# Performance work log

Hardware: AMD Instinct MI355X
Metric: run time of the kernel (lower is better)

The kernel has to match this reference:

```python
import jax, jax.numpy as jnp
import numpy as np

B, C_IN, H, W = 4, 512, 188, 188
SHARED_CH = 64
NUM_CLASS = 3
M = 200
NUM_MAX = 500
STRIDE = 8
PCR = (-75.2, -75.2, -2.0, 75.2, 75.2, 4.0)
VOX = (0.1, 0.1, 0.15)
OUT_CH = (2, 1, 3, 2, 1, 3)  # center, center_z, dim, rot, iou, hm
MIN_RADIUS = 2.0
OVERLAP = 0.1
INIT_BIAS = -2.19


def conv3x3(x, w):
    return jax.lax.conv_general_dilated(x, w, (1, 1), 'SAME',
                                        dimension_numbers=('NCHW', 'OIHW', 'NCHW'))


def bn_relu(x, p):
    # p: [4, C] = gamma, beta, running_mean, running_var (inference-mode BN)
    g, b, m, v = p[0], p[1], p[2], p[3]
    scale = (g * jax.lax.rsqrt(v + 1e-5))[None, :, None, None]
    y = (x - m[None, :, None, None]) * scale + b[None, :, None, None]
    return jax.nn.relu(y)


def gaussian_radius(height, width, min_overlap):
    # Faithful to OpenPCDet centernet_utils.gaussian_radius
    b1 = height + width
    c1 = width * height * (1 - min_overlap) / (1 + min_overlap)
    sq1 = jnp.sqrt(jnp.maximum(b1 * b1 - 4.0 * c1, 0.0))
    r1 = (b1 + sq1) / 2.0
    b2 = 2.0 * (height + width)
    c2 = (1 - min_overlap) * width * height
    sq2 = jnp.sqrt(jnp.maximum(b2 * b2 - 16.0 * c2, 0.0))
    r2 = (b2 + sq2) / 2.0
    a3 = 4.0 * min_overlap
    b3 = -2.0 * min_overlap * (height + width)
    c3 = (min_overlap - 1.0) * width * height
    sq3 = jnp.sqrt(jnp.maximum(b3 * b3 - 4.0 * a3 * c3, 0.0))
    r3 = (b3 + sq3) / 2.0
    return jnp.minimum(jnp.minimum(r1, r2), r3)


def assign_targets(gt_boxes):
    # gt_boxes: [B, M, 8] = x, y, z, dx, dy, dz, heading, class(1..NUM_CLASS)
    x, y, z = gt_boxes[..., 0], gt_boxes[..., 1], gt_boxes[..., 2]
    dx, dy, dz = gt_boxes[..., 3], gt_boxes[..., 4], gt_boxes[..., 5]
    heading = gt_boxes[..., 6]
    cls = jax.lax.stop_gradient(gt_boxes[..., 7]).astype(jnp.int32)

    cx = jnp.clip((x - PCR[0]) / VOX[0] / STRIDE, 0.0, W - 0.5)  # [B,M]
    cy = jnp.clip((y - PCR[1]) / VOX[1] / STRIDE, 0.0, H - 0.5)
    cxi = jax.lax.stop_gradient(jnp.floor(cx)).astype(jnp.int32)  # .int() trunc == floor (>=0)
    cyi = jax.lax.stop_gradient(jnp.floor(cy)).astype(jnp.int32)

    dxp = dx / VOX[0] / STRIDE
    dyp = dy / VOX[1] / STRIDE
    r = gaussian_radius(dxp, dyp, OVERLAP)
    r = jnp.maximum(jnp.floor(jax.lax.stop_gradient(r)), MIN_RADIUS)  # clamp_min(r.int(), 2)
    sigma = (2.0 * r + 1.0) / 6.0
    valid = (dx > 0) & (dy > 0)  # [B,M]

    ox = jnp.arange(W, dtype=jnp.int32)[None, None, :] - cxi[..., None]  # [B,M,W]
    oy = jnp.arange(H, dtype=jnp.int32)[None, None, :] - cyi[..., None]  # [B,M,H]
    d2 = (oy.astype(jnp.float32) ** 2)[:, :, :, None] + (ox.astype(jnp.float32) ** 2)[:, :, None, :]
    g = jnp.exp(-d2 / (2.0 * sigma * sigma)[:, :, None, None])  # [B,M,H,W]
    win = (jnp.abs(oy)[:, :, :, None] <= r[:, :, None, None]) & \
          (jnp.abs(ox)[:, :, None, :] <= r[:, :, None, None])
    g = jnp.where(win & valid[:, :, None, None], g, 0.0)

    # per-class max-splat (draw_gaussian_to_heatmap uses torch.max overlap)
    heatmap = jnp.stack(
        [jnp.max(jnp.where((cls == c + 1)[:, :, None, None], g, 0.0), axis=1)
         for c in range(NUM_CLASS)], axis=1)  # [B,NUM_CLASS,H,W]

    vf = valid.astype(gt_boxes.dtype)
    vals = jnp.stack([cx - cxi.astype(cx.dtype), cy - cyi.astype(cy.dtype), z,
                      jnp.log(dx), jnp.log(dy), jnp.log(dz),
                      jnp.cos(heading), jnp.sin(heading)], axis=-1) * vf[..., None]
    target_boxes = jnp.zeros((B, NUM_MAX, 8), gt_boxes.dtype).at[:, :M].set(vals)
    ind_vals = (cyi * W + cxi) * valid.astype(jnp.int32)
    inds = jnp.zeros((B, NUM_MAX), jnp.int32).at[:, :M].set(ind_vals)
    mask = jnp.zeros((B, NUM_MAX), jnp.int32).at[:, :M].set(valid.astype(jnp.int32))
    return heatmap, target_boxes, inds, mask


def setup_inputs() -> dict:
    key = jax.random.key(0)
    ks = jax.random.split(key, 16)
    spatial_features = jax.random.normal(ks[0], (B, C_IN, H, W), jnp.float32)
    x = jax.random.uniform(ks[1], (B, M), minval=-70.0, maxval=70.0)
    y = jax.random.uniform(ks[2], (B, M), minval=-70.0, maxval=70.0)
    z = jax.random.uniform(ks[3], (B, M), minval=-1.0, maxval=1.0)
    dx = jax.random.uniform(ks[4], (B, M), minval=1.5, maxval=5.0)
    dy = jax.random.uniform(ks[5], (B, M), minval=1.5, maxval=5.0)
    dz = jax.random.uniform(ks[6], (B, M), minval=1.0, maxval=3.0)
    hd = jax.random.uniform(ks[7], (B, M), minval=-np.pi, maxval=np.pi)
    cls = jax.random.randint(ks[8], (B, M), 1, NUM_CLASS + 1).astype(jnp.float32)
    gt_boxes = jnp.stack([x, y, z, dx, dy, dz, hd, cls], axis=-1)

    def mk_bn(k, lead):
        kk = jax.random.split(k, 4)
        g = 1.0 + 0.1 * jax.random.normal(kk[0], lead + (SHARED_CH,))
        b = 0.1 * jax.random.normal(kk[1], lead + (SHARED_CH,))
        m = 0.1 * jax.random.normal(kk[2], lead + (SHARED_CH,))
        v = jax.random.uniform(kk[3], lead + (SHARED_CH,), minval=0.5, maxval=1.5)
        return jnp.stack([g, b, m, v], axis=len(lead))

    w_shared = jax.random.normal(ks[9], (SHARED_CH, C_IN, 3, 3)) * (1.0 / np.sqrt(C_IN * 9))
    bn_shared = mk_bn(ks[10], ())
    w1_heads = jax.random.normal(ks[11], (6, SHARED_CH, SHARED_CH, 3, 3)) * (1.0 / np.sqrt(SHARED_CH * 9))
    bn_heads = mk_bn(ks[12], (6,))
    w2_heads = jax.random.normal(ks[13], (6, 3, SHARED_CH, 3, 3)) * (1.0 / np.sqrt(SHARED_CH * 9))
    b2_heads = jnp.zeros((6, 3), jnp.float32).at[5].set(INIT_BIAS)  # hm branch bias = -2.19
    return {'spatial_features': spatial_features, 'gt_boxes': gt_boxes,
            'w_shared': w_shared, 'bn_shared': bn_shared,
            'w1_heads': w1_heads, 'bn_heads': bn_heads,
            'w2_heads': w2_heads, 'b2_heads': b2_heads}


def reference(spatial_features, gt_boxes, w_shared, bn_shared,
              w1_heads, bn_heads, w2_heads, b2_heads):
    shared = bn_relu(conv3x3(spatial_features, w_shared), bn_shared)  # [B,64,H,W]

    def branch(w1, bnp, w2, b2):
        h = bn_relu(conv3x3(shared, w1), bnp)
        return conv3x3(h, w2) + b2[None, :, None, None]  # [B,3,H,W] (out padded to 3)

    outs = jax.vmap(branch)(w1_heads, bn_heads, w2_heads, b2_heads)  # [6,B,3,H,W]
    head_out = jnp.concatenate([outs[i, :, :OUT_CH[i]] for i in range(6)], axis=1)  # [B,12,H,W]

    heatmap, target_boxes, inds, mask = assign_targets(gt_boxes)
    return head_out, heatmap, target_boxes, inds, mask
```

## Files before the change

### kernel.cpp

```cpp
#include <hip/hip_runtime.h>
#include <hip/hip_bf16.h>

#define HWD 188
#define NPX (HWD*HWD)
#define NB 4
#define CIN 512
#define CH 64
#define MBOX 200
#define NMAX 500

#define HEAD_SZ (NB*12*NPX)
#define HM_OFF  HEAD_SZ
#define TB_OFF  (HM_OFF + NB*3*NPX)
#define IND_OFF (TB_OFF + NB*NMAX*8)
#define MSK_OFF (IND_OFF + NB*NMAX)

typedef short sh8 __attribute__((ext_vector_type(8)));
typedef float f4 __attribute__((ext_vector_type(4)));
typedef unsigned short us4 __attribute__((ext_vector_type(4)));

__device__ __constant__ int d_cum[6]  = {0, 2, 3, 6, 8, 9};
__device__ __constant__ int d_outc[6] = {2, 1, 3, 2, 1, 3};

__device__ __forceinline__ unsigned short bf16_bits(float v) {
  union { __hip_bfloat16 h; unsigned short u; } cv;
  cv.h = __float2bfloat16(v);
  return cv.u;
}

__device__ __forceinline__ int xcd_swz(int bid, int grid) {
  return (bid & 7) * (grid >> 3) + (bid >> 3);
}

__global__ __launch_bounds__(256) void wprep(
    const float* __restrict__ ws_, const float* __restrict__ w1_,
    const float* __restrict__ w2_, unsigned short* __restrict__ w1b,
    unsigned short* __restrict__ w2b, unsigned short* __restrict__ w3b) {
  int e = blockIdx.x * 256 + threadIdx.x;
  const int N1 = 9 * 16 * 64 * 32;
  const int N2 = 6 * 9 * 64 * 64;
  const int N3 = 6 * 9 * 16 * 64;
  if (e < N1) {
    int icr = e & 31; int r1 = e >> 5;
    int oc = r1 & 63; int r2 = r1 >> 6;
    int icq = r2 & 15; int tap = r2 >> 4;
    w1b[e] = bf16_bits(ws_[(oc * 512 + icq * 32 + icr) * 9 + tap]);
  } else if (e < N1 + N2) {
    int f = e - N1;
    int h = f / (9 * 64 * 64); int r = f % (9 * 64 * 64);
    int tap = r / (64 * 64); int r2 = r % (64 * 64);
    int oc = r2 / 64; int ic = r2 % 64;
    w2b[f] = bf16_bits(w1_[((h * 64 + oc) * 64 + ic) * 9 + tap]);
  } else if (e < N1 + N2 + N3) {
    int f = e - N1 - N2;
    int h = f / (9 * 16 * 64); int r = f % (9 * 16 * 64);
    int tap = r / (16 * 64); int r2 = r % (16 * 64);
    int oc = r2 / 64; int ic = r2 % 64;
    float v = (oc < 3) ? w2_[((h * 3 + oc) * 64 + ic) * 9 + tap] : 0.f;
    w3b[f] = bf16_bits(v);
  }
}

#define C1_LDS (10*18*32)
__global__ __launch_bounds__(256, 4) void conv1_mfma(
    const float* __restrict__ sf,
    const unsigned short* __restrict__ wb,
    const float* __restrict__ bnp,
    unsigned short* __restrict__ outp) {
  __shared__ __align__(16) short s_in[2][C1_LDS];
  const int t = threadIdx.x;
  const int swz = xcd_swz(blockIdx.x, 1152);
  const int b = swz / 288;
  const int tt = swz % 288;
  const int y0 = (tt / 12) * 8, x0 = (tt % 12) * 16;
  const int w = t >> 6, lane = t & 63, ln = lane & 15, kg = lane >> 4;
  const int rg = w & 1, og = w >> 1;

  const bool st_act = (t < 240);
  const int icg = t & 3, cg = (t >> 2) % 6, sr = (t >> 2) / 6;
  const int gy_s = y0 - 1 + sr;
  const int gx0_s = x0 - 4 + cg * 4;
  const bool row_ok = (gy_s >= 0 && gy_s < HWD);
  const bool vec_ok = (gx0_s >= 0 && gx0_s + 3 < HWD);
  const float* sbase = sf + (((long long)b * CIN + icg * 8) * HWD + gy_s) * HWD + gx0_s;

  f4 acc[2][4];
#pragma unroll
  for (int i = 0; i < 2; ++i)
#pragma unroll
    for (int j = 0; j < 4; ++j) acc[i][j] = (f4){0.f, 0.f, 0.f, 0.f};

  f4 st[8];
#pragma unroll
  for (int j = 0; j < 8; ++j) st[j] = (f4){0.f, 0.f, 0.f, 0.f};

#define C1_LOAD(IC0)                                                        \
  do {                                                                      \
    if (st_act && row_ok) {                                                 \
      const float* p = sbase + (long long)(IC0) * NPX;                      \
      if (vec_ok) {                                                         \
        _Pragma("unroll")                                                   \
        for (int j = 0; j < 8; ++j)                                         \
          st[j] = *reinterpret_cast<const f4*>(p + (long long)j * NPX);     \
      } else {                                                              \
        _Pragma("unroll")                                                   \
        for (int j = 0; j < 8; ++j) st[j] = (f4){0.f, 0.f, 0.f, 0.f};       \
        _Pragma("unroll")                                                   \
        for (int k = 0; k < 4; ++k) {                                       \
          int gx = gx0_s + k;                                               \
          if (gx >= 0 && gx < HWD) {                                        \
            _Pragma("unroll")                                               \
            for (int j = 0; j < 8; ++j) st[j][k] = p[(long long)j * NPX + k];\
          }                                                                 \
        }                                                                   \
      }                                                                     \
    } else {                                                                \
      _Pragma("unroll")                                                     \
      for (int j = 0; j < 8; ++j) st[j] = (f4){0.f, 0.f, 0.f, 0.f};         \
    }                                                                       \
  } while (0)

#define C1_WRITE(BUF)                                                       \
  do {                                                                      \
    if (st_act) {                                                           \
      _Pragma("unroll")                                                     \
      for (int k = 0; k < 4; ++k) {                                         \
        int col = cg * 4 + k - 3;                                           \
        if ((unsigned)col < 18u) {                                          \
          sh8 pk;                                                           \
          _Pragma("unroll")                                                 \
          for (int j = 0; j < 8; ++j) pk[j] = (short)bf16_bits(st[j][k]);   \
          *reinterpret_cast<sh8*>(&(BUF)[(sr * 18 + col) * 32 + icg * 8]) = pk; \
        }                                                                   \
      }                                                                     \
    }                                                                       \
  } while (0)

  C1_LOAD(0);
  C1_WRITE(s_in[0]);
  __syncthreads();

  for (int s = 0; s < 16; ++s) {
    const short* cur = s_in[s & 1];
    if (s < 15) C1_LOAD((s + 1) * 32);
#pragma unroll
    for (int tap = 0; tap < 9; ++tap) {
      const int ky = tap / 3, kx = tap % 3;
      sh8 af[2];
#pragma unroll
      for (int i = 0; i < 2; ++i)
        af[i] = *reinterpret_cast<const sh8*>(
            wb + (((tap * 16 + s) * 64) + (2 * og + i) * 16 + ln) * 32 + kg * 8);
#pragma unroll
      for (int nt = 0; nt < 4; ++nt) {
        const int rr = 4 * rg + nt + ky;
        const int cc = ln + kx;
        sh8 bf = *reinterpret_cast<const sh8*>(&cur[(rr * 18 + cc) * 32 + kg * 8]);
#pragma unroll
        for (int i = 0; i < 2; ++i)
          acc[i][nt] = __builtin_amdgcn_mfma_f32_16x16x32_bf16(
              af[i], bf, acc[i][nt], 0, 0, 0);
      }
    }
    if (s < 15) C1_WRITE(s_in[(s & 1) ^ 1]);
    __syncthreads();
  }

#pragma unroll
  for (int i = 0; i < 2; ++i) {
    const int ocb = (2 * og + i) * 16 + kg * 4;
    f4 g4 = *reinterpret_cast<const f4*>(bnp + ocb);
    f4 b4 = *reinterpret_cast<const f4*>(bnp + 64 + ocb);
    f4 m4 = *reinterpret_cast<const f4*>(bnp + 128 + ocb);
    f4 v4 = *reinterpret_cast<const f4*>(bnp + 192 + ocb);
    f4 sc, bi;
#pragma unroll
    for (int j = 0; j < 4; ++j) {
      sc[j] = g4[j] * rsqrtf(v4[j] + 1e-5f);
      bi[j] = b4[j] - m4[j] * sc[j];
    }
#pragma unroll
    for (int nt = 0; nt < 4; ++nt) {
      int y = y0 + 4 * rg + nt;
      int x = x0 + ln;
      if (y < HWD && x < HWD) {
        us4 pk;
#pragma unroll
        for (int j = 0; j < 4; ++j)
          pk[j] = bf16_bits(fmaxf(acc[i][nt][j] * sc[j] + bi[j], 0.f));
        *reinterpret_cast<us4*>(outp + (((long long)b * HWD + y) * HWD + x) * 64 + ocb) = pk;
      }
    }
  }
#undef C1_LOAD
#undef C1_WRITE
}

__global__ __launch_bounds__(256, 3) void conv2_allheads(
    const unsigned short* __restrict__ inp,
    const unsigned short* __restrict__ w2b,
    const float* __restrict__ bnH,
    unsigned short* __restrict__ tmp0,
    int h_lo, int h_hi, long long tstride) {
  __shared__ __align__(16) short s_in[10 * 34 * 72];
  const int t = threadIdx.x;
  const int swz = xcd_swz(blockIdx.x, gridDim.x);
  const int b = swz / 144;
  const int tt = swz % 144;
  const int y0 = (tt / 6) * 8, x0 = (tt % 6) * 32;
  const int w = t >> 6, lane = t & 63, ln = lane & 15, kg = lane >> 4;

  for (int idx = t; idx < 2720; idx += 256) {
    int ch = idx & 7; int pix = idx >> 3;
    int c = pix % 34; int r = pix / 34;
    int gy = y0 - 1 + r, gx = x0 - 1 + c;
    sh8 v = (sh8){0, 0, 0, 0, 0, 0, 0, 0};
    if (gy >= 0 && gy < HWD && gx >= 0 && gx < HWD)
      v = *reinterpret_cast<const sh8*>(
          &inp[(((long long)b * HWD + gy) * HWD + gx) * 64 + ch * 8]);
    *reinterpret_cast<sh8*>(&s_in[(r * 34 + c) * 72 + ch * 8]) = v;
  }
  __syncthreads();

  for (int h = h_lo; h < h_hi; ++h) {
    f4 acc[4][4];
#pragma unroll
    for (int i = 0; i < 4; ++i)
#pragma unroll
      for (int j = 0; j < 4; ++j) acc[i][j] = (f4){0.f, 0.f, 0.f, 0.f};
#pragma unroll
    for (int icq = 0; icq < 2; ++icq) {
#pragma unroll
      for (int tap = 0; tap < 9; ++tap) {
        const int ky = tap / 3, kx = tap % 3;
        sh8 af[4];
#pragma unroll
        for (int ot = 0; ot < 4; ++ot)
          af[ot] = *reinterpret_cast<const sh8*>(
              w2b + (((h * 9 + tap) * 64) + ot * 16 + ln) * 64 + icq * 32 + kg * 8);
#pragma unroll
        for (int nt = 0; nt < 4; ++nt) {
          const int rr = 2 * w + (nt >> 1) + ky;
          const int cc = (nt & 1) * 16 + ln + kx;
          sh8 bf = *reinterpret_cast<const sh8*>(
              &s_in[(rr * 34 + cc) * 72 + icq * 32 + kg * 8]);
#pragma unroll
          for (int ot = 0; ot < 4; ++ot)
            acc[ot][nt] = __builtin_amdgcn_mfma_f32_16x16x32_bf16(
                af[ot], bf, acc[ot][nt], 0, 0, 0);
        }
      }
    }
    unsigned short* outp = tmp0 + (long long)h * tstride;
    const float* bnp = bnH + h * 256;
#pragma unroll
    for (int ot = 0; ot < 4; ++ot) {
      const int ocb = ot * 16 + kg * 4;
      f4 g4 = *reinterpret_cast<const f4*>(bnp + ocb);
      f4 b4 = *reinterpret_cast<const f4*>(bnp + 64 + ocb);
      f4 m4 = *reinterpret_cast<const f4*>(bnp + 128 + ocb);
      f4 v4 = *reinterpret_cast<const f4*>(bnp + 192 + ocb);
      f4 sc, bi;
#pragma unroll
      for (int j = 0; j < 4; ++j) {
        sc[j] = g4[j] * rsqrtf(v4[j] + 1e-5f);
        bi[j] = b4[j] - m4[j] * sc[j];
      }
#pragma unroll
      for (int nt = 0; nt < 4; ++nt) {
        int y = y0 + 2 * w + (nt >> 1);
        int x = x0 + (nt & 1) * 16 + ln;
        if (y < HWD && x < HWD) {
          us4 pk;
#pragma unroll
          for (int j = 0; j < 4; ++j)
            pk[j] = bf16_bits(fmaxf(acc[ot][nt][j] * sc[j] + bi[j], 0.f));
          *reinterpret_cast<us4*>(outp + (((long long)b * HWD + y) * HWD + x) * 64 + ocb) = pk;
        }
      }
    }
  }
}

__global__ __launch_bounds__(256, 3) void conv3_mfma(
    const unsigned short* __restrict__ tmp0,
    const unsigned short* __restrict__ w3b,
    const float* __restrict__ b2,
    float* __restrict__ hout,
    int h_base, long long tstride) {
  __shared__ __align__(16) short s_in[10 * 34 * 72];
  const int t = threadIdx.x;
  const int swz = xcd_swz(blockIdx.x, gridDim.x);
  const int h = h_base + swz / 576;
  const int rem = swz % 576;
  const int b = rem / 144;
  const int tt = rem % 144;
  const int y0 = (tt / 6) * 8, x0 = (tt % 6) * 32;
  const int w = t >> 6, lane = t & 63, ln = lane & 15, kg = lane >> 4;
  const unsigned short* inp = tmp0 + (long long)h * tstride;

  for (int idx = t; idx < 2720; idx += 256) {
    int ch = idx & 7; int pix = idx >> 3;
    int c = pix % 34; int r = pix / 34;
    int gy = y0 - 1 + r, gx = x0 - 1 + c;
    sh8 v = (sh8){0, 0, 0, 0, 0, 0, 0, 0};
    if (gy >= 0 && gy < HWD && gx >= 0 && gx < HWD)
      v = *reinterpret_cast<const sh8*>(
          &inp[(((long long)b * HWD + gy) * HWD + gx) * 64 + ch * 8]);
    *reinterpret_cast<sh8*>(&s_in[(r * 34 + c) * 72 + ch * 8]) = v;
  }
  __syncthreads();

  f4 acc[4];
#pragma unroll
  for (int j = 0; j < 4; ++j) acc[j] = (f4){0.f, 0.f, 0.f, 0.f};
#pragma unroll
  for (int icq = 0; icq < 2; ++icq) {
#pragma unroll
    for (int tap = 0; tap < 9; ++tap) {
      const int ky = tap / 3, kx = tap % 3;
      sh8 af = *reinterpret_cast<const sh8*>(
          w3b + (((h * 9 + tap) * 16) + ln) * 64 + icq * 32 + kg * 8);
#pragma unroll
      for (int nt = 0; nt < 4; ++nt) {
        const int rr = 2 * w + (nt >> 1) + ky;
        const int cc = (nt & 1) * 16 + ln + kx;
        sh8 bf = *reinterpret_cast<const sh8*>(
            &s_in[(rr * 34 + cc) * 72 + icq * 32 + kg * 8]);
        acc[nt] = __builtin_amdgcn_mfma_f32_16x16x32_bf16(af, bf, acc[nt], 0, 0, 0);
      }
    }
  }
  const int c_off = d_cum[h], noc = d_outc[h];
#pragma unroll
  for (int nt = 0; nt < 4; ++nt) {
    int y = y0 + 2 * w + (nt >> 1);
    int x = x0 + (nt & 1) * 16 + ln;
    if (y < HWD && x < HWD) {
#pragma unroll
      for (int j = 0; j < 4; ++j) {
        int oc = kg * 4 + j;
        if (oc < noc)
          hout[((long long)b * 12 + c_off + oc) * NPX + y * HWD + x] =
              acc[nt][j] + b2[h * 3 + oc];
      }
    }
  }
}

__global__ __launch_bounds__(256) void targets_kernel(
    const float* __restrict__ gt, float* __restrict__ out, float* __restrict__ boxp) {
  int idx = blockIdx.x * 256 + threadIdx.x;
  if (idx >= NB * NMAX) return;
  int b = idx / NMAX, j = idx - b * NMAX;
  float vals[8] = {0, 0, 0, 0, 0, 0, 0, 0};
  float indf = 0.f, mkf = 0.f;
  if (j < MBOX) {
    const float* g = gt + (b * MBOX + j) * 8;
    float x = g[0], y = g[1], z = g[2], dx = g[3], dy = g[4], dz = g[5];
    float hd = g[6], cls = g[7];
    float cx = (x - (-75.2f)) / 0.1f / 8.0f;
    cx = fminf(fmaxf(cx, 0.0f), (float)HWD - 0.5f);
    float cy = (y - (-75.2f)) / 0.1f / 8.0f;
    cy = fminf(fmaxf(cy, 0.0f), (float)HWD - 0.5f);
    float cxf = floorf(cx), cyf = floorf(cy);
    int cxi = (int)cxf, cyi = (int)cyf;
    float hh = dx / 0.1f / 8.0f;
    float ww = dy / 0.1f / 8.0f;
    const float ov = 0.1f;
    float b1 = hh + ww;
    float c1 = ww * hh * (1.0f - ov) / (1.0f + ov);
    float sq1 = sqrtf(fmaxf(b1 * b1 - 4.0f * c1, 0.0f));
    float r1 = (b1 + sq1) / 2.0f;
    float b2_ = 2.0f * (hh + ww);
    float c2 = (1.0f - ov) * ww * hh;
    float sq2 = sqrtf(fmaxf(b2_ * b2_ - 16.0f * c2, 0.0f));
    float r2 = (b2_ + sq2) / 2.0f;
    float a3 = 4.0f * ov;
    float b3 = -2.0f * ov * (hh + ww);
    float c3 = (ov - 1.0f) * ww * hh;
    float sq3 = sqrtf(fmaxf(b3 * b3 - 4.0f * a3 * c3, 0.0f));
    float r3 = (b3 + sq3) / 2.0f;
    float r = fminf(fminf(r1, r2), r3);
    r = fmaxf(floorf(r), 2.0f);
    float sigma = (2.0f * r + 1.0f) / 6.0f;
    float inv2s2 = 1.0f / (2.0f * sigma * sigma);
    bool valid = (dx > 0.0f) && (dy > 0.0f);
    float vf = valid ? 1.0f : 0.0f;
    vals[0] = (cx - cxf) * vf;
    vals[1] = (cy - cyf) * vf;
    vals[2] = z * vf;
    vals[3] = logf(dx) * vf;
    vals[4] = logf(dy) * vf;
    vals[5] = logf(dz) * vf;
    vals[6] = cosf(hd) * vf;
    vals[7] = sinf(hd) * vf;
    indf = (float)((cyi * HWD + cxi) * (valid ? 1 : 0));
    mkf = vf;
    float* bp = boxp + (b * MBOX + j) * 8;
    bp[0] = cxf; bp[1] = cyf; bp[2] = r; bp[3] = inv2s2;
    bp[4] = valid ? cls : 0.0f; bp[5] = 0.f; bp[6] = 0.f; bp[7] = 0.f;
  }
  float* tb = out + TB_OFF + (b * NMAX + j) * 8;
#pragma unroll
  for (int k = 0; k < 8; ++k) tb[k] = vals[k];
  out[IND_OFF + b * NMAX + j] = indf;
  out[MSK_OFF + b * NMAX + j] = mkf;
}

__global__ __launch_bounds__(256) void heatmap_kernel(
    const float* __restrict__ boxp, float* __restrict__ out) {
  __shared__ float s_bp[MBOX][5];
  const int t = threadIdx.x, b = blockIdx.y;
  for (int e = t; e < MBOX * 5; e += 256) {
    int j = e / 5, k = e - j * 5;
    s_bp[j][k] = boxp[(b * MBOX + j) * 8 + k];
  }
  __syncthreads();
  int p = blockIdx.x * 256 + t;
  if (p >= NPX) return;
  int y = p / HWD, x = p - y * HWD;
  float a0 = 0.f, a1 = 0.f, a2 = 0.f;
  for (int j = 0; j < MBOX; ++j) {
    int c = (int)s_bp[j][4];
    if (c == 0) continue;
    float ox = (float)x - s_bp[j][0];
    float oy = (float)y - s_bp[j][1];
    float r = s_bp[j][2];
    if (fabsf(ox) <= r && fabsf(oy) <= r) {
      float gg = expf(-(ox * ox + oy * oy) * s_bp[j][3]);
      if (c == 1) a0 = fmaxf(a0, gg);
      else if (c == 2) a1 = fmaxf(a1, gg);
      else a2 = fmaxf(a2, gg);
    }
  }
  int base = HM_OFF + (b * 3 * HWD + y) * HWD + x;
  out[base] = a0;
  out[base + NPX] = a1;
  out[base + 2 * NPX] = a2;
}

extern "C" void kernel_launch(void* const* d_in, const int* in_sizes, int n_in,
                              void* d_out, int out_size, void* d_ws, size_t ws_size,
                              hipStream_t stream) {
  (void)in_sizes; (void)n_in; (void)out_size;
  const float* sf = (const float*)d_in[0];
  const float* gt = (const float*)d_in[1];
  const float* w_shared = (const float*)d_in[2];
  const float* bn_shared = (const float*)d_in[3];
  const float* w1 = (const float*)d_in[4];
  const float* bnH = (const float*)d_in[5];
  const float* w2 = (const float*)d_in[6];
  const float* b2 = (const float*)d_in[7];
  float* out = (float*)d_out;
  char* ws = (char*)d_ws;

  const size_t SH = (size_t)NB * NPX * 64 * 2;
  unsigned short* shared_t = (unsigned short*)ws;
  unsigned short* w1b = (unsigned short*)(ws + SH);
  unsigned short* w2b = (unsigned short*)(ws + SH + 589824);
  unsigned short* w3b = (unsigned short*)(ws + SH + 589824 + 442368);
  float* boxp = (float*)(ws + SH + 589824 + 442368 + 110592);
  const size_t off_tmp = SH + 589824 + 442368 + 110592 + 25600;
  unsigned short* tmp0 = (unsigned short*)(ws + off_tmp);

  const bool wide = ws_size >= off_tmp + 6 * SH;
  const long long tstride = wide ? (long long)(SH / 2) : 0LL;

  wprep<<<2232, 256, 0, stream>>>(w_shared, w1, w2, w1b, w2b, w3b);

  conv1_mfma<<<1152, 256, 0, stream>>>(sf, w1b, bn_shared, shared_t);

  if (wide) {
    conv2_allheads<<<576, 256, 0, stream>>>(shared_t, w2b, bnH, tmp0, 0, 6, tstride);
    conv3_mfma<<<3456, 256, 0, stream>>>(tmp0, w3b, b2, out, 0, tstride);
  } else {
    for (int h = 0; h < 6; ++h) {
      conv2_allheads<<<576, 256, 0, stream>>>(shared_t, w2b, bnH, tmp0, h, h + 1, 0);
      conv3_mfma<<<576, 256, 0, stream>>>(tmp0, w3b, b2, out, h, 0);
    }
  }

  targets_kernel<<<(NB * NMAX + 255) / 256, 256, 0, stream>>>(gt, out, boxp);
  heatmap_kernel<<<dim3((NPX + 255) / 256, NB), 256, 0, stream>>>(boxp, out);
}
```

Before: 686.6 us.

## Fuse per-head conv2 and conv3 into one kernel using LDS intermediate

Replaces the separate conv2 (all heads) and conv3 kernels with a single fused kernel. Each block handles one head on a 16x8 output tile. It computes the 18x10 haloed conv2 activation into shared memory, in two 32-channel halves, then runs the 3x3 conv3 from shared memory. This removes the global round trip of six bf16 64-channel intermediate tensors and one launch. In exchange it recomputes conv2 on halo pixels, reloads the shared input per head (6912 blocks), and tiles more finely with less weight reuse.

```diff
diff --git a/kernel.cpp b/kernel.cpp
--- a/kernel.cpp
+++ b/kernel.cpp
@@ -196,66 +196,95 @@
 #undef C1_WRITE
 }
 
-__global__ __launch_bounds__(256, 3) void conv2_allheads(
+__global__ __launch_bounds__(256, 3) void conv23_fused(
     const unsigned short* __restrict__ inp,
     const unsigned short* __restrict__ w2b,
+    const unsigned short* __restrict__ w3b,
     const float* __restrict__ bnH,
-    unsigned short* __restrict__ tmp0,
-    int h_lo, int h_hi, long long tstride) {
-  __shared__ __align__(16) short s_in[10 * 34 * 72];
+    const float* __restrict__ b2,
+    float* __restrict__ hout) {
+  __shared__ __align__(16) short s_in[240 * 72];
+  __shared__ __align__(16) short s_buf[180 * 36];
   const int t = threadIdx.x;
-  const int swz = xcd_swz(blockIdx.x, gridDim.x);
-  const int b = swz / 144;
-  const int tt = swz % 144;
-  const int y0 = (tt / 6) * 8, x0 = (tt % 6) * 32;
+  const int swz = xcd_swz(blockIdx.x, 6912);
+  const int h = swz % 6;
+  const int tile = swz / 6;
+  const int b = tile / 288;
+  const int tt = tile % 288;
+  const int y0 = (tt / 12) * 8, x0 = (tt % 12) * 16;
   const int w = t >> 6, lane = t & 63, ln = lane & 15, kg = lane >> 4;
 
-  for (int idx = t; idx < 2720; idx += 256) {
-    int ch = idx & 7; int pix = idx >> 3;
-    int c = pix % 34; int r = pix / 34;
-    int gy = y0 - 1 + r, gx = x0 - 1 + c;
+  for (int idx = t; idx < 1920; idx += 256) {
+    int ch8 = idx & 7; int px = idx >> 3;
+    int r = (px * 205) >> 12; int c = px - r * 20;
+    int gy = y0 - 2 + r, gx = x0 - 2 + c;
     sh8 v = (sh8){0, 0, 0, 0, 0, 0, 0, 0};
     if (gy >= 0 && gy < HWD && gx >= 0 && gx < HWD)
       v = *reinterpret_cast<const sh8*>(
-          &inp[(((long long)b * HWD + gy) * HWD + gx) * 64 + ch * 8]);
-    *reinterpret_cast<sh8*>(&s_in[(r * 34 + c) * 72 + ch * 8]) = v;
-  }
+          &inp[(((long long)b * HWD + gy) * HWD + gx) * 64 + ch8 * 8]);
+    *reinterpret_cast<sh8*>(&s_in[px * 72 + ch8 * 8]) = v;
+  }
+
+  int ibase[3];
+  int qaddr[3];
+  bool wr_ok[3];
+  bool img_ok[3];
+#pragma unroll
+  for (int nt = 0; nt < 3; ++nt) {
+    int q = (w * 3 + nt) * 16 + ln;
+    wr_ok[nt] = (q < 180);
+    if (q > 179) q = 179;
+    int r2 = (q * 57) >> 10; int c2 = q - r2 * 18;
+    ibase[nt] = (r2 * 20 + c2) * 72 + kg * 8;
+    qaddr[nt] = q;
+    int gy2 = y0 - 1 + r2, gx2 = x0 - 1 + c2;
+    img_ok[nt] = (gy2 >= 0 && gy2 < HWD && gx2 >= 0 && gx2 < HWD);
+  }
+  int b3base[2], oy[2], ox[2];
+#pragma unroll
+  for (int nt = 0; nt < 2; ++nt) {
+    int p = (w * 2 + nt) * 16 + ln;
+    int r3 = p >> 4, c3 = p & 15;
+    b3base[nt] = ((r3 + 1) * 18 + (c3 + 1)) * 36 + kg * 8;
+    oy[nt] = y0 + r3; ox[nt] = x0 + c3;
+  }
+
+  const float* bnp = bnH + h * 256;
+  f4 acc3[2];
+#pragma unroll
+  for (int j = 0; j < 2; ++j) acc3[j] = (f4){0.f, 0.f, 0.f, 0.f};
+
   __syncthreads();
 
-  for (int h = h_lo; h < h_hi; ++h) {
-    f4 acc[4][4];
-#pragma unroll
-    for (int i = 0; i < 4; ++i)
-#pragma unroll
-      for (int j = 0; j < 4; ++j) acc[i][j] = (f4){0.f, 0.f, 0.f, 0.f};
-#pragma unroll
+  for (int O = 0; O < 2; ++O) {
+    f4 acc2[2][3];
+#pragma unroll
+    for (int i = 0; i < 2; ++i)
+#pragma unroll
+      for (int j = 0; j < 3; ++j) acc2[i][j] = (f4){0.f, 0.f, 0.f, 0.f};
     for (int icq = 0; icq < 2; ++icq) {
 #pragma unroll
       for (int tap = 0; tap < 9; ++tap) {
         const int ky = tap / 3, kx = tap % 3;
-        sh8 af[4];
-#pragma unroll
-        for (int ot = 0; ot < 4; ++ot)
-          af[ot] = *reinterpret_cast<const sh8*>(
-              w2b + (((h * 9 + tap) * 64) + ot * 16 + ln) * 64 + icq * 32 + kg * 8);
-#pragma unroll
-        for (int nt = 0; nt < 4; ++nt) {
-          const int rr = 2 * w + (nt >> 1) + ky;
-          const int cc = (nt & 1) * 16 + ln + kx;
-          sh8 bf = *reinterpret_cast<const sh8*>(
-              &s_in[(rr * 34 + cc) * 72 + icq * 32 + kg * 8]);
-#pragma unroll
-          for (int ot = 0; ot < 4; ++ot)
-            acc[ot][nt] = __builtin_amdgcn_mfma_f32_16x16x32_bf16(
-                af[ot], bf, acc[ot][nt], 0, 0, 0);
+        const int toff = (ky * 20 + kx) * 72 + icq * 32;
+        sh8 af[2];
+#pragma unroll
+        for (int mt = 0; mt < 2; ++mt)
+          af[mt] = *reinterpret_cast<const sh8*>(
+              w2b + (((h * 9 + tap) * 64) + O * 32 + mt * 16 + ln) * 64 + icq * 32 + kg * 8);
+#pragma unroll
+        for (int nt = 0; nt < 3; ++nt) {
+          sh8 bf = *reinterpret_cast<const sh8*>(&s_in[ibase[nt] + toff]);
+#pragma unroll
+          for (int mt = 0; mt < 2; ++mt)
+            acc2[mt][nt] = __builtin_amdgcn_mfma_f32_16x16x32_bf16(
+                af[mt], bf, acc2[mt][nt], 0, 0, 0);
         }
       }
     }
-    unsigned short* outp = tmp0 + (long long)h * tstride;
-    const float* bnp = bnH + h * 256;
-#pragma unroll
-    for (int ot = 0; ot < 4; ++ot) {
-      const int ocb = ot * 16 + kg * 4;
+#pragma unroll
+    for (int mt = 0; mt < 2; ++mt) {
+      const int ocb = O * 32 + mt * 16 + kg * 4;
       f4 g4 = *reinterpret_cast<const f4*>(bnp + ocb);
       f4 b4 = *reinterpret_cast<const f4*>(bnp + 64 + ocb);
       f4 m4 = *reinterpret_cast<const f4*>(bnp + 128 + ocb);
@@ -267,82 +296,44 @@
         bi[j] = b4[j] - m4[j] * sc[j];
       }
 #pragma unroll
-      for (int nt = 0; nt < 4; ++nt) {
-        int y = y0 + 2 * w + (nt >> 1);
-        int x = x0 + (nt & 1) * 16 + ln;
-        if (y < HWD && x < HWD) {
-          us4 pk;
-#pragma unroll
-          for (int j = 0; j < 4; ++j)
-            pk[j] = bf16_bits(fmaxf(acc[ot][nt][j] * sc[j] + bi[j], 0.f));
-          *reinterpret_cast<us4*>(outp + (((long long)b * HWD + y) * HWD + x) * 64 + ocb) = pk;
+      for (int nt = 0; nt < 3; ++nt) {
+        if (wr_ok[nt]) {
+          us4 pk = {0, 0, 0, 0};
+          if (img_ok[nt]) {
+#pragma unroll
+            for (int j = 0; j < 4; ++j)
+              pk[j] = bf16_bits(fmaxf(acc2[mt][nt][j] * sc[j] + bi[j], 0.f));
+          }
+          *reinterpret_cast<us4*>(&s_buf[qaddr[nt] * 36 + mt * 16 + kg * 4]) = pk;
         }
       }
     }
-  }
-}
-
-__global__ __launch_bounds__(256, 3) void conv3_mfma(
-    const unsigned short* __restrict__ tmp0,
-    const unsigned short* __restrict__ w3b,
-    const float* __restrict__ b2,
-    float* __restrict__ hout,
-    int h_base, long long tstride) {
-  __shared__ __align__(16) short s_in[10 * 34 * 72];
-  const int t = threadIdx.x;
-  const int swz = xcd_swz(blockIdx.x, gridDim.x);
-  const int h = h_base + swz / 576;
-  const int rem = swz % 576;
-  const int b = rem / 144;
-  const int tt = rem % 144;
-  const int y0 = (tt / 6) * 8, x0 = (tt % 6) * 32;
-  const int w = t >> 6, lane = t & 63, ln = lane & 15, kg = lane >> 4;
-  const unsigned short* inp = tmp0 + (long long)h * tstride;
-
-  for (int idx = t; idx < 2720; idx += 256) {
-    int ch = idx & 7; int pix = idx >> 3;
-    int c = pix % 34; int r = pix / 34;
-    int gy = y0 - 1 + r, gx = x0 - 1 + c;
-    sh8 v = (sh8){0, 0, 0, 0, 0, 0, 0, 0};
-    if (gy >= 0 && gy < HWD && gx >= 0 && gx < HWD)
-      v = *reinterpret_cast<const sh8*>(
-          &inp[(((long long)b * HWD + gy) * HWD + gx) * 64 + ch * 8]);
-    *reinterpret_cast<sh8*>(&s_in[(r * 34 + c) * 72 + ch * 8]) = v;
-  }
-  __syncthreads();
-
-  f4 acc[4];
-#pragma unroll
-  for (int j = 0; j < 4; ++j) acc[j] = (f4){0.f, 0.f, 0.f, 0.f};
-#pragma unroll
-  for (int icq = 0; icq < 2; ++icq) {
+    __syncthreads();
 #pragma unroll
     for (int tap = 0; tap < 9; ++tap) {
-      const int ky = tap / 3, kx = tap % 3;
-      sh8 af = *reinterpret_cast<const sh8*>(
-          w3b + (((h * 9 + tap) * 16) + ln) * 64 + icq * 32 + kg * 8);
-#pragma unroll
-      for (int nt = 0; nt < 4; ++nt) {
-        const int rr = 2 * w + (nt >> 1) + ky;
-        const int cc = (nt & 1) * 16 + ln + kx;
-        sh8 bf = *reinterpret_cast<const sh8*>(
-            &s_in[(rr * 34 + cc) * 72 + icq * 32 + kg * 8]);
-        acc[nt] = __builtin_amdgcn_mfma_f32_16x16x32_bf16(af, bf, acc[nt], 0, 0, 0);
-      }
-    }
-  }
+      const int dy = tap / 3 - 1, dx = tap % 3 - 1;
+      const int toff = (dy * 18 + dx) * 36;
+      sh8 af3 = *reinterpret_cast<const sh8*>(
+          w3b + (((h * 9 + tap) * 16) + ln) * 64 + O * 32 + kg * 8);
+#pragma unroll
+      for (int nt = 0; nt < 2; ++nt) {
+        sh8 bf3 = *reinterpret_cast<const sh8*>(&s_buf[b3base[nt] + toff]);
+        acc3[nt] = __builtin_amdgcn_mfma_f32_16x16x32_bf16(af3, bf3, acc3[nt], 0, 0, 0);
+      }
+    }
+    __syncthreads();
+  }
+
   const int c_off = d_cum[h], noc = d_outc[h];
 #pragma unroll
-  for (int nt = 0; nt < 4; ++nt) {
-    int y = y0 + 2 * w + (nt >> 1);
-    int x = x0 + (nt & 1) * 16 + ln;
-    if (y < HWD && x < HWD) {
+  for (int nt = 0; nt < 2; ++nt) {
+    if (oy[nt] < HWD && ox[nt] < HWD) {
 #pragma unroll
       for (int j = 0; j < 4; ++j) {
         int oc = kg * 4 + j;
         if (oc < noc)
-          hout[((long long)b * 12 + c_off + oc) * NPX + y * HWD + x] =
-              acc[nt][j] + b2[h * 3 + oc];
+          hout[((long long)b * 12 + c_off + oc) * NPX + oy[nt] * HWD + ox[nt]] =
+              acc3[nt][j] + b2[h * 3 + oc];
       }
     }
   }
@@ -443,7 +434,7 @@
 extern "C" void kernel_launch(void* const* d_in, const int* in_sizes, int n_in,
                               void* d_out, int out_size, void* d_ws, size_t ws_size,
                               hipStream_t stream) {
-  (void)in_sizes; (void)n_in; (void)out_size;
+  (void)in_sizes; (void)n_in; (void)out_size; (void)ws_size;
   const float* sf = (const float*)d_in[0];
   const float* gt = (const float*)d_in[1];
   const float* w_shared = (const float*)d_in[2];
@@ -461,25 +452,12 @@
   unsigned short* w2b = (unsigned short*)(ws + SH + 589824);
   unsigned short* w3b = (unsigned short*)(ws + SH + 589824 + 442368);
   float* boxp = (float*)(ws + SH + 589824 + 442368 + 110592);
-  const size_t off_tmp = SH + 589824 + 442368 + 110592 + 25600;
-  unsigned short* tmp0 = (unsigned short*)(ws + off_tmp);
-
-  const bool wide = ws_size >= off_tmp + 6 * SH;
-  const long long tstride = wide ? (long long)(SH / 2) : 0LL;
 
   wprep<<<2232, 256, 0, stream>>>(w_shared, w1, w2, w1b, w2b, w3b);
 
   conv1_mfma<<<1152, 256, 0, stream>>>(sf, w1b, bn_shared, shared_t);
 
-  if (wide) {
-    conv2_allheads<<<576, 256, 0, stream>>>(shared_t, w2b, bnH, tmp0, 0, 6, tstride);
-    conv3_mfma<<<3456, 256, 0, stream>>>(tmp0, w3b, b2, out, 0, tstride);
-  } else {
-    for (int h = 0; h < 6; ++h) {
-      conv2_allheads<<<576, 256, 0, stream>>>(shared_t, w2b, bnH, tmp0, h, h + 1, 0);
-      conv3_mfma<<<576, 256, 0, stream>>>(tmp0, w3b, b2, out, h, 0);
-    }
-  }
+  conv23_fused<<<6912, 256, 0, stream>>>(shared_t, w2b, w3b, bnH, b2, out);
 
   targets_kernel<<<(NB * NMAX + 255) / 256, 256, 0, stream>>>(gt, out, boxp);
   heatmap_kernel<<<dim3((NPX + 255) / 256, NB), 256, 0, stream>>>(boxp, out);
```

After: 594.8 us. 1.15x faster.
